# Performance work log

Measured on AMD Instinct MI355X. Metric: run time of the kernel, lower is better.

Reference implementation:

```python
import jax, jax.numpy as jnp
import numpy as np

L, T, H, F = 16, 2048, 2048, 512  # layers, tokens (B*S=16*128), hidden, features


def setup_inputs() -> dict:
    key = jax.random.key(0)
    k1, k2, k3 = jax.random.split(key, 3)
    x = jax.random.normal(k1, (L, T, H), dtype=jnp.float32)          # stacked residual activations
    W_enc = jax.random.normal(k2, (L, F, H), dtype=jnp.float32) * 0.02  # per-layer encoder (out,in)
    # Dense pack of decoders: W_dec[s, t] is the (source s -> target t) decoder weight (H, F).
    # Only entries with s <= t exist in the original ModuleDict; others are masked to zero in reference().
    W_dec = jax.random.normal(k3, (L, L, H, F), dtype=jnp.float32) * 0.02
    return {"x": x, "W_enc": W_enc, "W_dec": W_dec}


def reference(x, W_enc, W_dec):
    n_layers = x.shape[0]
    # encode: feature_activations[l] = JumpReLU(x[l] @ W_enc[l].T), threshold=0 -> relu
    feats = jax.nn.relu(jnp.einsum('sth,sfh->stf', x, W_enc))  # [L, T, F]
    # causal mask over (source s, target l): decoder exists iff s <= l
    tri = jnp.tril(jnp.ones((n_layers, n_layers), x.dtype))     # tri[l, s] = 1 if s <= l
    Wd = W_dec * tri.T[:, :, None, None]                        # zero out s > l entries
    # reconstruction[l] = sum_{s<=l} feats[s] @ W_dec[s,l].T  (single blocked contraction)
    recon = jnp.einsum('stf,slhf->lth', feats, Wd)              # [L, T, H]
    return feats, recon
```

## Files before the change

kernel.cpp:

```cpp
#include <hip/hip_runtime.h>

#define NL 16
#define NT 2048
#define NH 2048
#define NF 512
#define NPAIR 136

typedef short bf16x8 __attribute__((ext_vector_type(8)));
typedef float f32x4 __attribute__((ext_vector_type(4)));
typedef short s16x4 __attribute__((ext_vector_type(4)));

__device__ __forceinline__ short f2bf(float f) {
  union { float f; unsigned u; } x; x.f = f;
  unsigned r = (x.u + 0x7fffu + ((x.u >> 16) & 1u)) >> 16;
  return (short)r;
}

__device__ __forceinline__ int imin(int a, int b) { return a < b ? a : b; }


__global__ void k_cvt_f32_bf16(const float* __restrict__ src, short* __restrict__ dst, int n4) {
  int i = blockIdx.x * blockDim.x + threadIdx.x;
  const int stride = gridDim.x * blockDim.x;
  for (; i < n4; i += stride) {
    const float4 v = reinterpret_cast<const float4*>(src)[i];
    s16x4 o;
    o[0] = f2bf(v.x); o[1] = f2bf(v.y); o[2] = f2bf(v.z); o[3] = f2bf(v.w);
    reinterpret_cast<s16x4*>(dst)[i] = o;
  }
}

__global__ void k_cvt_wdec(const float* __restrict__ wdec, short* __restrict__ dst) {
  const int p = blockIdx.y;
  int l = 0;
  while ((l + 1) * (l + 2) / 2 <= p) ++l;
  const int s = p - l * (l + 1) / 2;
  const float* src = wdec + (size_t)(s * NL + l) * (NH * NF);
  short* d = dst + (size_t)p * (NH * NF);
  const int n4 = NH * NF / 4;
  for (int i = blockIdx.x * blockDim.x + threadIdx.x; i < n4; i += gridDim.x * blockDim.x) {
    const float4 v = reinterpret_cast<const float4*>(src)[i];
    s16x4 o;
    o[0] = f2bf(v.x); o[1] = f2bf(v.y); o[2] = f2bf(v.z); o[3] = f2bf(v.w);
    reinterpret_cast<s16x4*>(d)[i] = o;
  }
}


__device__ __forceinline__ bf16x8 lds_frag(const short* slot, int r, int cbyte) {
  int byte = (r << 7) + cbyte;
  byte ^= (r & 7) << 4;
  return *reinterpret_cast<const bf16x8*>(reinterpret_cast<const char*>(slot) + byte);
}

__device__ __forceinline__ void stage_half(short* slot, const short* gbase, int ld,
                                           int isA, int h, int tid, int wave) {
#pragma unroll
  for (int j = 0; j < 2; ++j) {
    const int o = j * 8192 + tid * 16;
    const int r = o >> 7;
    const int cb = (o ^ ((r & 7) << 4)) & 127;
    const int g = isA ? (((r >> 6) << 7) + h * 64 + (r & 63))
                      : (((r >> 5) << 6) + h * 32 + (r & 31));
    __builtin_amdgcn_global_load_lds(
        (const __attribute__((address_space(1))) void*)(gbase + (size_t)g * ld + (cb >> 1)),
        (__attribute__((address_space(3))) void*)((char*)slot + j * 8192 + wave * 1024),
        16, 0, 0);
  }
}

__device__ __forceinline__ void stage_tile(short (*buf)[8192], const short* At,
                                           const short* Bt, int lda, int ldb,
                                           int tid, int wave) {
  stage_half(buf[0], At, lda, 1, 0, tid, wave);
  stage_half(buf[1], At, lda, 1, 1, tid, wave);
  stage_half(buf[2], Bt, ldb, 0, 0, tid, wave);
  stage_half(buf[3], Bt, ldb, 0, 1, tid, wave);
}

template <typename SFn>
__device__ __forceinline__ void ktile_flat(short (*bufc)[8192], f32x4 (&acc)[2][2][4][2],
                                           int wr, int wc, int lane, SFn stagefn) {
  const int lr = lane & 15;
  const int ko = (lane >> 4) * 16;
  stagefn();
  bf16x8 b0[2][2], b1[2][2], a0[2][4], a1[2][4];
#pragma unroll
  for (int kk = 0; kk < 2; ++kk) {
#pragma unroll
    for (int n = 0; n < 2; ++n) {
      b0[kk][n] = lds_frag(bufc[2], wc * 32 + n * 16 + lr, kk * 64 + ko);
      b1[kk][n] = lds_frag(bufc[3], wc * 32 + n * 16 + lr, kk * 64 + ko);
    }
#pragma unroll
    for (int m = 0; m < 4; ++m)
      a0[kk][m] = lds_frag(bufc[0], wr * 64 + m * 16 + lr, kk * 64 + ko);
  }
  __builtin_amdgcn_s_setprio(1);
#pragma unroll
  for (int kk = 0; kk < 2; ++kk)
#pragma unroll
    for (int m = 0; m < 4; ++m)
#pragma unroll
      for (int n = 0; n < 2; ++n) {
        acc[0][0][m][n] = __builtin_amdgcn_mfma_f32_16x16x32_bf16(a0[kk][m], b0[kk][n],
                                                                  acc[0][0][m][n], 0, 0, 0);
        acc[0][1][m][n] = __builtin_amdgcn_mfma_f32_16x16x32_bf16(a0[kk][m], b1[kk][n],
                                                                  acc[0][1][m][n], 0, 0, 0);
      }
  __builtin_amdgcn_s_setprio(0);
#pragma unroll
  for (int kk = 0; kk < 2; ++kk)
#pragma unroll
    for (int m = 0; m < 4; ++m)
      a1[kk][m] = lds_frag(bufc[1], wr * 64 + m * 16 + lr, kk * 64 + ko);
  __builtin_amdgcn_s_setprio(1);
#pragma unroll
  for (int kk = 0; kk < 2; ++kk)
#pragma unroll
    for (int m = 0; m < 4; ++m)
#pragma unroll
      for (int n = 0; n < 2; ++n) {
        acc[1][0][m][n] = __builtin_amdgcn_mfma_f32_16x16x32_bf16(a1[kk][m], b0[kk][n],
                                                                  acc[1][0][m][n], 0, 0, 0);
        acc[1][1][m][n] = __builtin_amdgcn_mfma_f32_16x16x32_bf16(a1[kk][m], b1[kk][n],
                                                                  acc[1][1][m][n], 0, 0, 0);
      }
  __builtin_amdgcn_s_setprio(0);
  asm volatile("s_waitcnt vmcnt(0) lgkmcnt(0)" ::: "memory");
  __builtin_amdgcn_s_barrier();
}


__global__ __launch_bounds__(512, 2) void k_encode256(const short* __restrict__ xbf,
                                                      const short* __restrict__ webf,
                                                      float* __restrict__ feats_f32,
                                                      short* __restrict__ feats_bf) {
  __shared__ short lds[2][4][8192];
  const int l = blockIdx.z;
  const int row0 = blockIdx.y * 256;
  const int col0 = blockIdx.x * 256;
  const int tid = threadIdx.x;
  const int wave = tid >> 6, lane = tid & 63;
  const int wr = wave >> 2, wc = wave & 3;

  const short* A = xbf + (size_t)l * NT * NH + (size_t)row0 * NH;
  const short* B = webf + (size_t)l * NF * NH + (size_t)col0 * NH;

  f32x4 acc[2][2][4][2];
#pragma unroll
  for (int qa = 0; qa < 2; ++qa)
#pragma unroll
    for (int qb = 0; qb < 2; ++qb)
#pragma unroll
      for (int m = 0; m < 4; ++m)
#pragma unroll
        for (int n = 0; n < 2; ++n) {
          f32x4 z = {0.f, 0.f, 0.f, 0.f};
          acc[qa][qb][m][n] = z;
        }

  const int KT = NH / 64;
  stage_tile(lds[0], A, B, NH, NH, tid, wave);
  asm volatile("s_waitcnt vmcnt(0)" ::: "memory");
  __builtin_amdgcn_s_barrier();

  for (int u = 0; u < KT; ++u) {
    short(*bufc)[8192] = lds[u & 1];
    short(*bufn)[8192] = lds[(u + 1) & 1];
    ktile_flat(bufc, acc, wr, wc, lane, [&] {
      if (u + 1 < KT)
        stage_tile(bufn, A + (u + 1) * 64, B + (u + 1) * 64, NH, NH, tid, wave);
    });
  }

  const int lr4 = (lane >> 4) * 4, lc = lane & 15;
  float* outF = feats_f32 + (size_t)l * NT * NF;
  short* outB = feats_bf + (size_t)l * NT * NF;
#pragma unroll
  for (int qa = 0; qa < 2; ++qa)
#pragma unroll
    for (int qb = 0; qb < 2; ++qb)
#pragma unroll
      for (int m = 0; m < 4; ++m)
#pragma unroll
        for (int n = 0; n < 2; ++n)
#pragma unroll
          for (int rg = 0; rg < 4; ++rg) {
            const int rr = row0 + wr * 128 + qa * 64 + m * 16 + lr4 + rg;
            const int cc = col0 + wc * 64 + qb * 32 + n * 16 + lc;
            float v = acc[qa][qb][m][n][rg];
            v = v > 0.f ? v : 0.f;
            outF[(size_t)rr * NF + cc] = v;
            outB[(size_t)rr * NF + cc] = f2bf(v);
          }
}


__global__ __launch_bounds__(512, 2) void k_decode256(const short* __restrict__ featsbf,
                                                      const short* __restrict__ wdbf,
                                                      float* __restrict__ recon) {
  __shared__ short lds[2][4][8192];
  const int l = (NL - 1) - blockIdx.z;
  const int row0 = blockIdx.y * 256;
  const int col0 = blockIdx.x * 256;
  const int tid = threadIdx.x;
  const int wave = tid >> 6, lane = tid & 63;
  const int wr = wave >> 2, wc = wave & 3;
  const int pbase = l * (l + 1) / 2;

  const short* Af = featsbf + (size_t)row0 * NF;
  const short* Bw = wdbf + (size_t)col0 * NF;

  f32x4 acc[2][2][4][2];
#pragma unroll
  for (int qa = 0; qa < 2; ++qa)
#pragma unroll
    for (int qb = 0; qb < 2; ++qb)
#pragma unroll
      for (int m = 0; m < 4; ++m)
#pragma unroll
        for (int n = 0; n < 2; ++n) {
          f32x4 z = {0.f, 0.f, 0.f, 0.f};
          acc[qa][qb][m][n] = z;
        }

  const int KT = 8 * (l + 1);
#define ABASE(kt) (Af + (size_t)((kt) >> 3) * (NT * NF) + ((kt)&7) * 64)
#define BBASE(kt) (Bw + (size_t)(pbase + ((kt) >> 3)) * (NH * NF) + ((kt)&7) * 64)

  stage_tile(lds[0], ABASE(0), BBASE(0), NF, NF, tid, wave);
  asm volatile("s_waitcnt vmcnt(0)" ::: "memory");
  __builtin_amdgcn_s_barrier();

  for (int u = 0; u < KT; ++u) {
    short(*bufc)[8192] = lds[u & 1];
    short(*bufn)[8192] = lds[(u + 1) & 1];
    ktile_flat(bufc, acc, wr, wc, lane, [&] {
      if (u + 1 < KT)
        stage_tile(bufn, ABASE(u + 1), BBASE(u + 1), NF, NF, tid, wave);
    });
  }
#undef ABASE
#undef BBASE

  const int lr4 = (lane >> 4) * 4, lc = lane & 15;
  float* out = recon + (size_t)l * NT * NH;
#pragma unroll
  for (int qa = 0; qa < 2; ++qa)
#pragma unroll
    for (int qb = 0; qb < 2; ++qb)
#pragma unroll
      for (int m = 0; m < 4; ++m)
#pragma unroll
        for (int n = 0; n < 2; ++n)
#pragma unroll
          for (int rg = 0; rg < 4; ++rg) {
            const int rr = row0 + wr * 128 + qa * 64 + m * 16 + lr4 + rg;
            const int cc = col0 + wc * 64 + qb * 32 + n * 16 + lc;
            out[(size_t)rr * NH + cc] = acc[qa][qb][m][n][rg];
          }
}


extern "C" void kernel_launch(void* const* d_in, const int* in_sizes, int n_in,
                              void* d_out, int out_size, void* d_ws, size_t ws_size,
                              hipStream_t stream) {
  const float* x = (const float*)d_in[0];
  const float* wenc = (const float*)d_in[1];
  const float* wdec = (const float*)d_in[2];

  float* feats_f32 = (float*)d_out;
  float* recon = feats_f32 + (size_t)NL * NT * NF;

  short* x_bf = (short*)d_ws;
  short* we_bf = x_bf + (size_t)NL * NT * NH;
  short* wd_bf = we_bf + (size_t)NL * NF * NH;
  short* ft_bf = wd_bf + (size_t)NPAIR * NH * NF;

  k_cvt_f32_bf16<<<2048, 256, 0, stream>>>(x, x_bf, NL * NT * NH / 4);
  k_cvt_f32_bf16<<<2048, 256, 0, stream>>>(wenc, we_bf, NL * NF * NH / 4);
  k_cvt_wdec<<<dim3(512, NPAIR), 256, 0, stream>>>(wdec, wd_bf);

  k_encode256<<<dim3(2, 8, 16), 512, 0, stream>>>(x_bf, we_bf, feats_f32, ft_bf);
  k_decode256<<<dim3(8, 8, 16), 512, 0, stream>>>(ft_bf, wd_bf, recon);
}
```

Before: 821.1 us.

## Fuse fp32-to-bf16 conversion of x and W_dec into GEMM tile staging

```diff
diff --git a/kernel.cpp b/kernel.cpp
--- a/kernel.cpp
+++ b/kernel.cpp
@@ -9,6 +9,7 @@
 typedef short bf16x8 __attribute__((ext_vector_type(8)));
 typedef float f32x4 __attribute__((ext_vector_type(4)));
 typedef short s16x4 __attribute__((ext_vector_type(4)));
+typedef unsigned u32x4 __attribute__((ext_vector_type(4)));
 
 __device__ __forceinline__ short f2bf(float f) {
   union { float f; unsigned u; } x; x.f = f;
@@ -16,7 +17,11 @@
   return (short)r;
 }
 
-__device__ __forceinline__ int imin(int a, int b) { return a < b ? a : b; }
+__device__ __forceinline__ unsigned cvtpk(float a, float b) {
+  unsigned r;
+  asm("v_cvt_pk_bf16_f32 %0, %1, %2" : "=v"(r) : "v"(a), "v"(b));
+  return r;
+}
 
 
 __global__ void k_cvt_f32_bf16(const float* __restrict__ src, short* __restrict__ dst, int n4) {
@@ -27,22 +32,6 @@
     s16x4 o;
     o[0] = f2bf(v.x); o[1] = f2bf(v.y); o[2] = f2bf(v.z); o[3] = f2bf(v.w);
     reinterpret_cast<s16x4*>(dst)[i] = o;
-  }
-}
-
-__global__ void k_cvt_wdec(const float* __restrict__ wdec, short* __restrict__ dst) {
-  const int p = blockIdx.y;
-  int l = 0;
-  while ((l + 1) * (l + 2) / 2 <= p) ++l;
-  const int s = p - l * (l + 1) / 2;
-  const float* src = wdec + (size_t)(s * NL + l) * (NH * NF);
-  short* d = dst + (size_t)p * (NH * NF);
-  const int n4 = NH * NF / 4;
-  for (int i = blockIdx.x * blockDim.x + threadIdx.x; i < n4; i += gridDim.x * blockDim.x) {
-    const float4 v = reinterpret_cast<const float4*>(src)[i];
-    s16x4 o;
-    o[0] = f2bf(v.x); o[1] = f2bf(v.y); o[2] = f2bf(v.z); o[3] = f2bf(v.w);
-    reinterpret_cast<s16x4*>(d)[i] = o;
   }
 }
 
@@ -69,21 +58,41 @@
   }
 }
 
-__device__ __forceinline__ void stage_tile(short (*buf)[8192], const short* At,
-                                           const short* Bt, int lda, int ldb,
-                                           int tid, int wave) {
-  stage_half(buf[0], At, lda, 1, 0, tid, wave);
-  stage_half(buf[1], At, lda, 1, 1, tid, wave);
-  stage_half(buf[2], Bt, ldb, 0, 0, tid, wave);
-  stage_half(buf[3], Bt, ldb, 0, 1, tid, wave);
-}
-
-template <typename SFn>
+struct F32Half { float4 q[2][2]; };
+
+__device__ __forceinline__ void issue_f32half(F32Half& st, const float* gbase, int ld,
+                                              int isA, int h, int tid) {
+#pragma unroll
+  for (int j = 0; j < 2; ++j) {
+    const int o = j * 8192 + tid * 16;
+    const int r = o >> 7;
+    const int cb = (o ^ ((r & 7) << 4)) & 127;
+    const int g = isA ? (((r >> 6) << 7) + h * 64 + (r & 63))
+                      : (((r >> 5) << 6) + h * 32 + (r & 31));
+    const float* p = gbase + (size_t)g * ld + (cb >> 1);
+    st.q[j][0] = *reinterpret_cast<const float4*>(p);
+    st.q[j][1] = *reinterpret_cast<const float4*>(p + 4);
+  }
+}
+
+__device__ __forceinline__ void commit_f32half(const F32Half& st, short* slot, int tid) {
+#pragma unroll
+  for (int j = 0; j < 2; ++j) {
+    u32x4 o;
+    o[0] = cvtpk(st.q[j][0].x, st.q[j][0].y);
+    o[1] = cvtpk(st.q[j][0].z, st.q[j][0].w);
+    o[2] = cvtpk(st.q[j][1].x, st.q[j][1].y);
+    o[3] = cvtpk(st.q[j][1].z, st.q[j][1].w);
+    *reinterpret_cast<u32x4*>((char*)slot + j * 8192 + tid * 16) = o;
+  }
+}
+
+template <typename IFn, typename CFn>
 __device__ __forceinline__ void ktile_flat(short (*bufc)[8192], f32x4 (&acc)[2][2][4][2],
-                                           int wr, int wc, int lane, SFn stagefn) {
+                                           int wr, int wc, int lane, IFn issue, CFn commit) {
   const int lr = lane & 15;
   const int ko = (lane >> 4) * 16;
-  stagefn();
+  issue();
   bf16x8 b0[2][2], b1[2][2], a0[2][4], a1[2][4];
 #pragma unroll
   for (int kk = 0; kk < 2; ++kk) {
@@ -127,12 +136,13 @@
                                                                   acc[1][1][m][n], 0, 0, 0);
       }
   __builtin_amdgcn_s_setprio(0);
+  commit();
   asm volatile("s_waitcnt vmcnt(0) lgkmcnt(0)" ::: "memory");
   __builtin_amdgcn_s_barrier();
 }
 
 
-__global__ __launch_bounds__(512, 2) void k_encode256(const short* __restrict__ xbf,
+__global__ __launch_bounds__(512, 2) void k_encode256(const float* __restrict__ xf,
                                                       const short* __restrict__ webf,
                                                       float* __restrict__ feats_f32,
                                                       short* __restrict__ feats_bf) {
@@ -144,7 +154,7 @@
   const int wave = tid >> 6, lane = tid & 63;
   const int wr = wave >> 2, wc = wave & 3;
 
-  const short* A = xbf + (size_t)l * NT * NH + (size_t)row0 * NH;
+  const float* A = xf + (size_t)l * NT * NH + (size_t)row0 * NH;
   const short* B = webf + (size_t)l * NF * NH + (size_t)col0 * NH;
 
   f32x4 acc[2][2][4][2];
@@ -161,17 +171,34 @@
         }
 
   const int KT = NH / 64;
-  stage_tile(lds[0], A, B, NH, NH, tid, wave);
-  asm volatile("s_waitcnt vmcnt(0)" ::: "memory");
+  F32Half stA0, stA1;
+  issue_f32half(stA0, A, NH, 1, 0, tid);
+  issue_f32half(stA1, A, NH, 1, 1, tid);
+  stage_half(lds[0][2], B, NH, 0, 0, tid, wave);
+  stage_half(lds[0][3], B, NH, 0, 1, tid, wave);
+  commit_f32half(stA0, lds[0][0], tid);
+  commit_f32half(stA1, lds[0][1], tid);
+  asm volatile("s_waitcnt vmcnt(0) lgkmcnt(0)" ::: "memory");
   __builtin_amdgcn_s_barrier();
 
   for (int u = 0; u < KT; ++u) {
     short(*bufc)[8192] = lds[u & 1];
     short(*bufn)[8192] = lds[(u + 1) & 1];
-    ktile_flat(bufc, acc, wr, wc, lane, [&] {
-      if (u + 1 < KT)
-        stage_tile(bufn, A + (u + 1) * 64, B + (u + 1) * 64, NH, NH, tid, wave);
-    });
+    ktile_flat(bufc, acc, wr, wc, lane,
+        [&] {
+          if (u + 1 < KT) {
+            issue_f32half(stA0, A + (u + 1) * 64, NH, 1, 0, tid);
+            issue_f32half(stA1, A + (u + 1) * 64, NH, 1, 1, tid);
+            stage_half(bufn[2], B + (u + 1) * 64, NH, 0, 0, tid, wave);
+            stage_half(bufn[3], B + (u + 1) * 64, NH, 0, 1, tid, wave);
+          }
+        },
+        [&] {
+          if (u + 1 < KT) {
+            commit_f32half(stA0, bufn[0], tid);
+            commit_f32half(stA1, bufn[1], tid);
+          }
+        });
   }
 
   const int lr4 = (lane >> 4) * 4, lc = lane & 15;
@@ -198,7 +225,7 @@
 
 
 __global__ __launch_bounds__(512, 2) void k_decode256(const short* __restrict__ featsbf,
-                                                      const short* __restrict__ wdbf,
+                                                      const float* __restrict__ wdecf,
                                                       float* __restrict__ recon) {
   __shared__ short lds[2][4][8192];
   const int l = (NL - 1) - blockIdx.z;
@@ -207,10 +234,9 @@
   const int tid = threadIdx.x;
   const int wave = tid >> 6, lane = tid & 63;
   const int wr = wave >> 2, wc = wave & 3;
-  const int pbase = l * (l + 1) / 2;
 
   const short* Af = featsbf + (size_t)row0 * NF;
-  const short* Bw = wdbf + (size_t)col0 * NF;
+  const float* Bw = wdecf + (size_t)col0 * NF;
 
   f32x4 acc[2][2][4][2];
 #pragma unroll
@@ -227,22 +253,39 @@
 
   const int KT = 8 * (l + 1);
 #define ABASE(kt) (Af + (size_t)((kt) >> 3) * (NT * NF) + ((kt)&7) * 64)
-#define BBASE(kt) (Bw + (size_t)(pbase + ((kt) >> 3)) * (NH * NF) + ((kt)&7) * 64)
-
-  stage_tile(lds[0], ABASE(0), BBASE(0), NF, NF, tid, wave);
-  asm volatile("s_waitcnt vmcnt(0)" ::: "memory");
+#define BBASEF(kt) (Bw + (size_t)(((kt) >> 3) * NL + l) * (NH * NF) + ((kt)&7) * 64)
+
+  F32Half stB0, stB1;
+  stage_half(lds[0][0], ABASE(0), NF, 1, 0, tid, wave);
+  stage_half(lds[0][1], ABASE(0), NF, 1, 1, tid, wave);
+  issue_f32half(stB0, BBASEF(0), NF, 0, 0, tid);
+  issue_f32half(stB1, BBASEF(0), NF, 0, 1, tid);
+  commit_f32half(stB0, lds[0][2], tid);
+  commit_f32half(stB1, lds[0][3], tid);
+  asm volatile("s_waitcnt vmcnt(0) lgkmcnt(0)" ::: "memory");
   __builtin_amdgcn_s_barrier();
 
   for (int u = 0; u < KT; ++u) {
     short(*bufc)[8192] = lds[u & 1];
     short(*bufn)[8192] = lds[(u + 1) & 1];
-    ktile_flat(bufc, acc, wr, wc, lane, [&] {
-      if (u + 1 < KT)
-        stage_tile(bufn, ABASE(u + 1), BBASE(u + 1), NF, NF, tid, wave);
-    });
+    ktile_flat(bufc, acc, wr, wc, lane,
+        [&] {
+          if (u + 1 < KT) {
+            stage_half(bufn[0], ABASE(u + 1), NF, 1, 0, tid, wave);
+            stage_half(bufn[1], ABASE(u + 1), NF, 1, 1, tid, wave);
+            issue_f32half(stB0, BBASEF(u + 1), NF, 0, 0, tid);
+            issue_f32half(stB1, BBASEF(u + 1), NF, 0, 1, tid);
+          }
+        },
+        [&] {
+          if (u + 1 < KT) {
+            commit_f32half(stB0, bufn[2], tid);
+            commit_f32half(stB1, bufn[3], tid);
+          }
+        });
   }
 #undef ABASE
-#undef BBASE
+#undef BBASEF
 
   const int lr4 = (lane >> 4) * 4, lc = lane & 15;
   float* out = recon + (size_t)l * NT * NH;
@@ -273,15 +316,11 @@
   float* feats_f32 = (float*)d_out;
   float* recon = feats_f32 + (size_t)NL * NT * NF;
 
-  short* x_bf = (short*)d_ws;
-  short* we_bf = x_bf + (size_t)NL * NT * NH;
-  short* wd_bf = we_bf + (size_t)NL * NF * NH;
-  short* ft_bf = wd_bf + (size_t)NPAIR * NH * NF;
-
-  k_cvt_f32_bf16<<<2048, 256, 0, stream>>>(x, x_bf, NL * NT * NH / 4);
-  k_cvt_f32_bf16<<<2048, 256, 0, stream>>>(wenc, we_bf, NL * NF * NH / 4);
-  k_cvt_wdec<<<dim3(512, NPAIR), 256, 0, stream>>>(wdec, wd_bf);
-
-  k_encode256<<<dim3(2, 8, 16), 512, 0, stream>>>(x_bf, we_bf, feats_f32, ft_bf);
-  k_decode256<<<dim3(8, 8, 16), 512, 0, stream>>>(ft_bf, wd_bf, recon);
-}
+  short* we_bf = (short*)d_ws;
+  short* ft_bf = we_bf + (size_t)NL * NF * NH;
+
+  k_cvt_f32_bf16<<<1024, 256, 0, stream>>>(wenc, we_bf, NL * NF * NH / 4);
+
+  k_encode256<<<dim3(2, 8, 16), 512, 0, stream>>>(x, we_bf, feats_f32, ft_bf);
+  k_decode256<<<dim3(8, 8, 16), 512, 0, stream>>>(ft_bf, wdec, recon);
+}
```

New measurement: 1.169 ms. 1.42x slower.
